# Kernel optimization log

Measured on AMD Instinct MI355X. Metric: run time of the kernel, lower is better.

## Reference

```python
import jax, jax.numpy as jnp
import numpy as np

N_HEAD = 16
ROPE_BASE = 10000.0


def _rope_tables(T, head_dim, dtype):
    inv_freq = 1.0 / (ROPE_BASE ** (jnp.arange(0, head_dim, 2, dtype=jnp.float32) / head_dim))
    t = jnp.arange(T, dtype=jnp.float32)
    freqs = t[:, None] * inv_freq[None, :]          # [T, hd/2]
    emb = jnp.concatenate([freqs, freqs], axis=-1)  # [T, hd]
    return jnp.cos(emb).astype(dtype), jnp.sin(emb).astype(dtype)


def _rotate_half(x):
    h = x.shape[-1] // 2
    return jnp.concatenate([-x[..., h:], x[..., :h]], axis=-1)


def setup_inputs() -> dict:
    key = jax.random.key(0)
    k1, k2, k3 = jax.random.split(key, 3)
    B, T, C = 2, 2048, 1024
    x = jax.random.normal(k1, (B, T, C), dtype=jnp.float32)
    w_attn = jax.random.normal(k2, (3 * C, C), dtype=jnp.float32) * (1.0 / np.sqrt(C))
    w_proj = jax.random.normal(k3, (C, C), dtype=jnp.float32) * (1.0 / np.sqrt(C))
    return {"x": x, "w_attn": w_attn, "w_proj": w_proj}


def reference(x, w_attn, w_proj):
    B, T, C = x.shape
    H = N_HEAD
    hd = C // H

    qkv = jnp.einsum('btc,fc->btf', x, w_attn)          # [B,T,3C]
    q, k, v = jnp.split(qkv, 3, axis=-1)
    # [B,H,T,hd]
    q = q.reshape(B, T, H, hd).transpose(0, 2, 1, 3)
    k = k.reshape(B, T, H, hd).transpose(0, 2, 1, 3)
    v = v.reshape(B, T, H, hd).transpose(0, 2, 1, 3)

    cos, sin = _rope_tables(T, hd, x.dtype)             # [T,hd]
    cos = cos[None, None]
    sin = sin[None, None]
    q = q * cos + _rotate_half(q) * sin
    k = k * cos + _rotate_half(k) * sin

    scale = 1.0 / np.sqrt(hd)
    scores = jnp.einsum('bhqd,bhkd->bhqk', q, k) * scale  # [B,H,T,T]
    causal = jnp.tril(jnp.ones((T, T), dtype=bool))
    scores = jnp.where(causal[None, None], scores, jnp.finfo(scores.dtype).min)
    attn = jax.nn.softmax(scores, axis=-1)
    out = jnp.einsum('bhqk,bhkd->bhqd', attn, v)          # [B,H,T,hd]
    out = out.transpose(0, 2, 1, 3).reshape(B, T, C)
    return jnp.einsum('btc,oc->bto', out, w_proj)
```

## Files before the change

kernel.cpp:

```cpp
#include <hip/hip_runtime.h>
#include <hip/hip_bf16.h>
#include <stdint.h>

typedef unsigned short u16;
typedef __bf16 bf16x8 __attribute__((ext_vector_type(8)));
typedef float f32x4 __attribute__((ext_vector_type(4)));

#define B_ 2
#define T_ 2048
#define C_ 1024
#define H_ 16
#define HD 64
#define M_ (B_ * T_)
#define N3 (3 * C_)

__device__ __forceinline__ float bf2f(u16 u) {
  return __uint_as_float(((unsigned int)u) << 16);
}
__device__ __forceinline__ u16 f2bf(float f) {
  unsigned int u = __float_as_uint(f);
  u += 0x7FFF + ((u >> 16) & 1);
  return (u16)(u >> 16);
}
__device__ __forceinline__ unsigned cvt_pk_bf16(float lo, float hi) {
  unsigned r;
  asm("v_cvt_pk_bf16_f32 %0, %1, %2" : "=v"(r) : "v"(lo), "v"(hi));
  return r;
}
__device__ __forceinline__ void async16(void* ldsp, const void* gp) {
  __builtin_amdgcn_global_load_lds(
      (const __attribute__((address_space(1))) unsigned int*)gp,
      (__attribute__((address_space(3))) unsigned int*)ldsp, 16, 0, 0);
}

union U16x8 { uint4 v; u16 u[8]; };

__device__ __forceinline__ bf16x8 ldsAfrag(const char* base, int row, int kbyte) {
  int off = (row * 128 + kbyte) ^ ((row & 7) << 4);
  uint4 t = *reinterpret_cast<const uint4*>(base + off);
  return __builtin_bit_cast(bf16x8, t);
}
__device__ __forceinline__ bf16x8 ldsAfrag256(const char* base, int row, int kbyte) {
  int off = (row * 256 + kbyte) ^ ((row & 7) << 4);
  uint4 t = *reinterpret_cast<const uint4*>(base + off);
  return __builtin_bit_cast(bf16x8, t);
}

__global__ void cvt_bf16(const float* __restrict__ src, u16* __restrict__ dst, int n4) {
  int i = blockIdx.x * blockDim.x + threadIdx.x;
  int stride = gridDim.x * blockDim.x;
  for (; i < n4; i += stride) {
    float4 v = reinterpret_cast<const float4*>(src)[i];
    uint2 o;
    o.x = (unsigned)f2bf(v.x) | ((unsigned)f2bf(v.y) << 16);
    o.y = (unsigned)f2bf(v.z) | ((unsigned)f2bf(v.w) << 16);
    reinterpret_cast<uint2*>(dst)[i] = o;
  }
}

__global__ void rope_tables_kernel(float* __restrict__ cosT, float* __restrict__ sinT) {
  int t = blockIdx.x;
  int i = threadIdx.x;
  float inv = powf(10000.0f, -(float)i * (1.0f / 32.0f));
  float f = (float)t * inv;
  cosT[t * 32 + i] = cosf(f);
  sinT[t * 32 + i] = sinf(f);
}

template <bool OUT_F32>
__global__ __launch_bounds__(256) void gemm_bt(const u16* __restrict__ A,
                                               const u16* __restrict__ Bw,
                                               void* __restrict__ Cout,
                                               int M, int N, int K) {
  __shared__ uint4 ldsbuf[2048];
  char* As = (char*)ldsbuf;
  char* Bs = (char*)ldsbuf + 16384;
  const int tid = threadIdx.x;
  const int lane = tid & 63;
  const int wv = tid >> 6;
  const int wr = wv >> 1, wc = wv & 1;
  const int lrow = lane & 15, lgrp = lane >> 4;
  const long m0 = (long)blockIdx.x * 128, n0 = (long)blockIdx.y * 128;
  const int srow = tid >> 3, sc = tid & 7;
  f32x4 acc[4][4] = {};
  for (int k0 = 0; k0 < K; k0 += 64) {
    __syncthreads();
#pragma unroll
    for (int p = 0; p < 4; ++p) {
      int row = srow + p * 32;
      uint4 va = *reinterpret_cast<const uint4*>(A + (m0 + row) * K + k0 + sc * 8);
      *reinterpret_cast<uint4*>(As + ((row * 128 + sc * 16) ^ ((row & 7) << 4))) = va;
      uint4 vb = *reinterpret_cast<const uint4*>(Bw + (n0 + row) * K + k0 + sc * 8);
      *reinterpret_cast<uint4*>(Bs + ((row * 128 + sc * 16) ^ ((row & 7) << 4))) = vb;
    }
    __syncthreads();
#pragma unroll
    for (int ks = 0; ks < 2; ++ks) {
      bf16x8 af[4], bfr[4];
#pragma unroll
      for (int i = 0; i < 4; ++i) {
        af[i]  = ldsAfrag(As, wr * 64 + i * 16 + lrow, ks * 64 + lgrp * 16);
        bfr[i] = ldsAfrag(Bs, wc * 64 + i * 16 + lrow, ks * 64 + lgrp * 16);
      }
#pragma unroll
      for (int i = 0; i < 4; ++i)
#pragma unroll
        for (int j = 0; j < 4; ++j)
          acc[i][j] = __builtin_amdgcn_mfma_f32_16x16x32_bf16(af[i], bfr[j], acc[i][j], 0, 0, 0);
    }
  }
#pragma unroll
  for (int i = 0; i < 4; ++i)
#pragma unroll
    for (int j = 0; j < 4; ++j) {
      long r0 = m0 + wr * 64 + i * 16 + lgrp * 4;
      long c  = n0 + wc * 64 + j * 16 + lrow;
#pragma unroll
      for (int r = 0; r < 4; ++r) {
        float v = acc[i][j][r];
        if (OUT_F32)
          ((float*)Cout)[(r0 + r) * N + c] = v;
        else
          ((u16*)Cout)[(r0 + r) * N + c] = f2bf(v);
      }
    }
}

__global__ __launch_bounds__(256) void rope_reshape(const u16* __restrict__ qkv,
                                                    const float* __restrict__ cosT,
                                                    const float* __restrict__ sinT,
                                                    u16* __restrict__ Q,
                                                    u16* __restrict__ K,
                                                    u16* __restrict__ Vt) {
  __shared__ u16 Vs[64][80];
  const int tid = threadIdx.x;
  const int tblk = blockIdx.x, bh = blockIdx.y;
  const int b = bh >> 4, h = bh & 15;
  const int tl = tid >> 2, quar = tid & 3;
  const int t = tblk * 64 + tl;
  const u16* rowp = qkv + ((size_t)(b * T_ + t)) * N3 + h * HD;
  const int d0 = quar * 8;
  float cs[8], sn[8];
#pragma unroll
  for (int j = 0; j < 8; ++j) {
    cs[j] = cosT[t * 32 + d0 + j];
    sn[j] = sinT[t * 32 + d0 + j];
  }
#pragma unroll
  for (int part = 0; part < 2; ++part) {
    const u16* p = rowp + part * C_;
    U16x8 x1, x2, o1, o2;
    x1.v = *reinterpret_cast<const uint4*>(p + d0);
    x2.v = *reinterpret_cast<const uint4*>(p + d0 + 32);
#pragma unroll
    for (int j = 0; j < 8; ++j) {
      float a = bf2f(x1.u[j]), c2 = bf2f(x2.u[j]);
      o1.u[j] = f2bf(a * cs[j] - c2 * sn[j]);
      o2.u[j] = f2bf(c2 * cs[j] + a * sn[j]);
    }
    u16* dst = (part ? K : Q) + ((size_t)bh * T_ + t) * HD;
    *reinterpret_cast<uint4*>(dst + d0) = o1.v;
    *reinterpret_cast<uint4*>(dst + d0 + 32) = o2.v;
  }
  const u16* pv = rowp + 2 * C_;
#pragma unroll
  for (int c = 0; c < 2; ++c) {
    int d = quar * 16 + c * 8;
    *reinterpret_cast<uint4*>(&Vs[tl][d]) = *reinterpret_cast<const uint4*>(pv + d);
  }
  __syncthreads();
  const int d = tid >> 2, tq = tid & 3;
  U16x8 a, bv;
#pragma unroll
  for (int j = 0; j < 8; ++j) a.u[j] = Vs[tq * 16 + j][d];
#pragma unroll
  for (int j = 0; j < 8; ++j) bv.u[j] = Vs[tq * 16 + 8 + j][d];
  u16* dstv = Vt + ((size_t)bh * HD + d) * T_ + tblk * 64 + tq * 16;
  *reinterpret_cast<uint4*>(dstv) = a.v;
  *reinterpret_cast<uint4*>(dstv + 8) = bv.v;
}

__global__ __launch_bounds__(256) void attn_fwd7(const u16* __restrict__ Q,
                                                 const u16* __restrict__ K,
                                                 const u16* __restrict__ Vt,
                                                 u16* __restrict__ O) {
  __shared__ uint4 lds4[5120];
  char* ldsb = (char*)lds4;
  const int tid = threadIdx.x;
  const int lane = tid & 63, wv = tid >> 6;
  const int lrow = lane & 15, lgrp = lane >> 4;
  char* Ps = ldsb + 65536 + wv * 4096;
  const int bh = blockIdx.y;
  const int b = bh >> 4, h = bh & 15;
  const u16* Qh = Q + (size_t)bh * T_ * HD;
  const u16* Kh = K + (size_t)bh * T_ * HD;
  const u16* Vh = Vt + (size_t)bh * HD * T_;

  const int kc_src = ((lane & 7) ^ (lane >> 3)) * 8;
  const int krow_l = lane >> 3;
  const int vrow_l = lane >> 4;

  auto stage = [&](int bufsel, int k0s) {
    char* Kd = ldsb + (bufsel << 15);
    char* Vd = Kd + 16384;
    const u16* Kg = Kh + (size_t)k0s * HD;
    const u16* Vg = Vh + k0s;
#pragma unroll
    for (int seg = 0; seg < 4; ++seg) {
      const u16* gk = Kg + (size_t)(wv * 32 + seg * 8 + krow_l) * HD + kc_src;
      async16(Kd + wv * 4096 + seg * 1024, gk);
      int d = wv * 16 + seg * 4 + vrow_l;
      const u16* gv = Vg + (size_t)d * T_ + ((lane & 15) ^ (d & 7)) * 8;
      async16(Vd + wv * 4096 + seg * 1024, gv);
    }
  };

  const float SCL = 0.125f * 1.44269504089f;
  const float CBIAS = 16.0f;
  uint4 ones4;
  ones4.x = ones4.y = ones4.z = ones4.w = 0x3F803F80u;
  const bf16x8 ones8 = __builtin_bit_cast(bf16x8, ones4);
  int cur = 0;

#pragma unroll
  for (int uu = 0; uu < 2; ++uu) {
    const int unit = uu ? (31 - (int)blockIdx.x) : (int)blockIdx.x;
    const int qs = unit * 64;
    const int q_glob = qs + wv * 16 + lrow;
    bf16x8 qf[2];
#pragma unroll
    for (int ks = 0; ks < 2; ++ks) {
      uint4 t4 = *reinterpret_cast<const uint4*>(
          Qh + (size_t)(qs + wv * 16 + lrow) * HD + ks * 32 + lgrp * 8);
      qf[ks] = __builtin_bit_cast(bf16x8, t4);
    }
    f32x4 o[4] = {};
    f32x4 lacc = {};
    const int niter = (unit >> 1) + 1;

    stage(cur, 0);
    __syncthreads();

    for (int kt = 0; kt < niter; ++kt) {
      const int k0 = kt * 128;
      if (kt + 1 < niter) stage(cur ^ 1, k0 + 128);
      char* Ksb = ldsb + (cur << 15);
      char* Vsb = Ksb + 16384;

      f32x4 s[8] = {};
      __builtin_amdgcn_s_setprio(1);
#pragma unroll
      for (int ks = 0; ks < 2; ++ks)
#pragma unroll
        for (int n = 0; n < 8; ++n) {
          bf16x8 bk = ldsAfrag(Ksb, n * 16 + lrow, ks * 64 + lgrp * 16);
          s[n] = __builtin_amdgcn_mfma_f32_16x16x32_bf16(bk, qf[ks], s[n], 0, 0, 0);
        }
      __builtin_amdgcn_s_setprio(0);

      const bool diag = (kt == niter - 1);
#pragma unroll
      for (int n = 0; n < 8; ++n)
#pragma unroll
        for (int r = 0; r < 4; ++r) {
          float v = __builtin_fmaf(s[n][r], SCL, -CBIAS);
          if (diag) {
            int kg = k0 + n * 16 + lgrp * 4 + r;
            v = (kg <= q_glob) ? v : -__builtin_inff();
          }
          s[n][r] = exp2f(v);
        }

#pragma unroll
      for (int n = 0; n < 8; ++n) {
        uint2 w;
        w.x = cvt_pk_bf16(s[n][0], s[n][1]);
        w.y = cvt_pk_bf16(s[n][2], s[n][3]);
        int off = (lrow * 256 + n * 32 + lgrp * 8) ^ ((lrow & 7) << 4);
        *reinterpret_cast<uint2*>(Ps + off) = w;
      }

      __builtin_amdgcn_s_setprio(1);
#pragma unroll
      for (int ks = 0; ks < 4; ++ks) {
        bf16x8 pa = ldsAfrag256(Ps, lrow, ks * 64 + lgrp * 16);
        lacc = __builtin_amdgcn_mfma_f32_16x16x32_bf16(pa, ones8, lacc, 0, 0, 0);
#pragma unroll
        for (int dn = 0; dn < 4; ++dn) {
          bf16x8 bv = ldsAfrag256(Vsb, dn * 16 + lrow, ks * 64 + lgrp * 16);
          o[dn] = __builtin_amdgcn_mfma_f32_16x16x32_bf16(pa, bv, o[dn], 0, 0, 0);
        }
      }
      __builtin_amdgcn_s_setprio(0);
      __syncthreads();
      cur ^= 1;
    }

#pragma unroll
    for (int r = 0; r < 4; ++r) {
      float inv = 1.0f / lacc[r];
      int t = qs + wv * 16 + lgrp * 4 + r;
#pragma unroll
      for (int dn = 0; dn < 4; ++dn) {
        int c = h * HD + dn * 16 + lrow;
        O[((size_t)(b * T_ + t)) * C_ + c] = f2bf(o[dn][r] * inv);
      }
    }
  }
}

extern "C" void kernel_launch(void* const* d_in, const int* in_sizes, int n_in,
                              void* d_out, int out_size, void* d_ws, size_t ws_size,
                              hipStream_t stream) {
  const float* x  = (const float*)d_in[0];
  const float* wa = (const float*)d_in[1];
  const float* wp = (const float*)d_in[2];
  float* out = (float*)d_out;
  char* ws = (char*)d_ws;
  size_t off = 0;
  auto alloc = [&](size_t bytes) {
    char* p = ws + off;
    off += (bytes + 255) & ~(size_t)255;
    return p;
  };
  u16* xb   = (u16*)alloc((size_t)M_ * C_ * 2);
  u16* wab  = (u16*)alloc((size_t)N3 * C_ * 2);
  u16* wpb  = (u16*)alloc((size_t)C_ * C_ * 2);
  u16* qkvb = (u16*)alloc((size_t)M_ * N3 * 2);
  u16* Qb   = (u16*)alloc((size_t)B_ * H_ * T_ * HD * 2);
  u16* Kb   = (u16*)alloc((size_t)B_ * H_ * T_ * HD * 2);
  u16* Vtb  = (u16*)alloc((size_t)B_ * H_ * T_ * HD * 2);
  u16* Ob   = (u16*)alloc((size_t)M_ * C_ * 2);
  float* cosT = (float*)alloc((size_t)T_ * 32 * 4);
  float* sinT = (float*)alloc((size_t)T_ * 32 * 4);
  (void)in_sizes; (void)n_in; (void)out_size; (void)ws_size;

  cvt_bf16<<<1024, 256, 0, stream>>>(x, xb, M_ * C_ / 4);
  cvt_bf16<<<1024, 256, 0, stream>>>(wa, wab, N3 * C_ / 4);
  cvt_bf16<<<512, 256, 0, stream>>>(wp, wpb, C_ * C_ / 4);
  rope_tables_kernel<<<T_, 32, 0, stream>>>(cosT, sinT);
  gemm_bt<false><<<dim3(M_ / 128, N3 / 128), 256, 0, stream>>>(xb, wab, qkvb, M_, N3, C_);
  rope_reshape<<<dim3(T_ / 64, B_ * H_), 256, 0, stream>>>(qkvb, cosT, sinT, Qb, Kb, Vtb);
  attn_fwd7<<<dim3(16, B_ * H_), 256, 0, stream>>>(Qb, Kb, Vtb, Ob);
  gemm_bt<true><<<dim3(M_ / 128, C_ / 128), 256, 0, stream>>>(Ob, wpb, out, M_, C_, C_);
}
```

Baseline: 131.5 us.

## Use async LDS loads in GEMM, fold softmax scale into Q, precompute attention LDS addresses

After: 128.0 us. 1.03x faster.

```diff
diff --git a/kernel.cpp b/kernel.cpp
--- a/kernel.cpp
+++ b/kernel.cpp
@@ -40,9 +40,8 @@
   uint4 t = *reinterpret_cast<const uint4*>(base + off);
   return __builtin_bit_cast(bf16x8, t);
 }
-__device__ __forceinline__ bf16x8 ldsAfrag256(const char* base, int row, int kbyte) {
-  int off = (row * 256 + kbyte) ^ ((row & 7) << 4);
-  uint4 t = *reinterpret_cast<const uint4*>(base + off);
+__device__ __forceinline__ bf16x8 ldsRead(const char* p) {
+  uint4 t = *reinterpret_cast<const uint4*>(p);
   return __builtin_bit_cast(bf16x8, t);
 }
 
@@ -81,17 +80,17 @@
   const int wr = wv >> 1, wc = wv & 1;
   const int lrow = lane & 15, lgrp = lane >> 4;
   const long m0 = (long)blockIdx.x * 128, n0 = (long)blockIdx.y * 128;
-  const int srow = tid >> 3, sc = tid & 7;
+  const int srow_l = lane >> 3;
+  const int csrc = ((lane & 7) ^ (lane >> 3)) * 8;
   f32x4 acc[4][4] = {};
   for (int k0 = 0; k0 < K; k0 += 64) {
     __syncthreads();
 #pragma unroll
     for (int p = 0; p < 4; ++p) {
-      int row = srow + p * 32;
-      uint4 va = *reinterpret_cast<const uint4*>(A + (m0 + row) * K + k0 + sc * 8);
-      *reinterpret_cast<uint4*>(As + ((row * 128 + sc * 16) ^ ((row & 7) << 4))) = va;
-      uint4 vb = *reinterpret_cast<const uint4*>(Bw + (n0 + row) * K + k0 + sc * 8);
-      *reinterpret_cast<uint4*>(Bs + ((row * 128 + sc * 16) ^ ((row & 7) << 4))) = vb;
+      int seg = wv * 4 + p;
+      int row = seg * 8 + srow_l;
+      async16(As + seg * 1024, A + (size_t)(m0 + row) * K + k0 + csrc);
+      async16(Bs + seg * 1024, Bw + (size_t)(n0 + row) * K + k0 + csrc);
     }
     __syncthreads();
 #pragma unroll
@@ -133,6 +132,7 @@
                                                     u16* __restrict__ K,
                                                     u16* __restrict__ Vt) {
   __shared__ u16 Vs[64][80];
+  const float SCLQ = 0.125f * 1.4426950408889634f;
   const int tid = threadIdx.x;
   const int tblk = blockIdx.x, bh = blockIdx.y;
   const int b = bh >> 4, h = bh & 15;
@@ -155,8 +155,11 @@
 #pragma unroll
     for (int j = 0; j < 8; ++j) {
       float a = bf2f(x1.u[j]), c2 = bf2f(x2.u[j]);
-      o1.u[j] = f2bf(a * cs[j] - c2 * sn[j]);
-      o2.u[j] = f2bf(c2 * cs[j] + a * sn[j]);
+      float f1 = a * cs[j] - c2 * sn[j];
+      float f2 = c2 * cs[j] + a * sn[j];
+      if (part == 0) { f1 *= SCLQ; f2 *= SCLQ; }
+      o1.u[j] = f2bf(f1);
+      o2.u[j] = f2bf(f2);
     }
     u16* dst = (part ? K : Q) + ((size_t)bh * T_ + t) * HD;
     *reinterpret_cast<uint4*>(dst + d0) = o1.v;
@@ -180,7 +183,7 @@
   *reinterpret_cast<uint4*>(dstv + 8) = bv.v;
 }
 
-__global__ __launch_bounds__(256) void attn_fwd7(const u16* __restrict__ Q,
+__global__ __launch_bounds__(256) void attn_fwd8(const u16* __restrict__ Q,
                                                  const u16* __restrict__ K,
                                                  const u16* __restrict__ Vt,
                                                  u16* __restrict__ O) {
@@ -215,8 +218,18 @@
     }
   };
 
-  const float SCL = 0.125f * 1.44269504089f;
-  const float CBIAS = 16.0f;
+  const int swz = (lrow & 7) << 4;
+  const int kread_a = lrow * 128 + ((lgrp * 16) ^ swz);
+  const int kread_b = lrow * 128 + ((64 + lgrp * 16) ^ swz);
+  const int vread_a = 16384 + lrow * 256 + ((lgrp * 16) ^ swz);
+  const int vread_b = 16384 + lrow * 256 + ((64 + lgrp * 16) ^ swz);
+  const char* pa_a = Ps + lrow * 256 + ((lgrp * 16) ^ swz);
+  const char* pa_b = Ps + lrow * 256 + ((64 + lgrp * 16) ^ swz);
+  char* pw0 = Ps + lrow * 256 + (((0 * 32 + lgrp * 8)) ^ swz);
+  char* pw1 = Ps + lrow * 256 + (((1 * 32 + lgrp * 8)) ^ swz);
+  char* pw2 = Ps + lrow * 256 + (((2 * 32 + lgrp * 8)) ^ swz);
+  char* pw3 = Ps + lrow * 256 + (((3 * 32 + lgrp * 8)) ^ swz);
+
   uint4 ones4;
   ones4.x = ones4.y = ones4.z = ones4.w = 0x3F803F80u;
   const bf16x8 ones8 = __builtin_bit_cast(bf16x8, ones4);
@@ -244,50 +257,58 @@
     for (int kt = 0; kt < niter; ++kt) {
       const int k0 = kt * 128;
       if (kt + 1 < niter) stage(cur ^ 1, k0 + 128);
-      char* Ksb = ldsb + (cur << 15);
-      char* Vsb = Ksb + 16384;
+      const char* Kb = ldsb + (cur << 15);
+      const char* KbA = Kb + kread_a;
+      const char* KbB = Kb + kread_b;
+      const char* VbA = Kb + vread_a;
+      const char* VbB = Kb + vread_b;
 
       f32x4 s[8] = {};
       __builtin_amdgcn_s_setprio(1);
 #pragma unroll
-      for (int ks = 0; ks < 2; ++ks)
-#pragma unroll
-        for (int n = 0; n < 8; ++n) {
-          bf16x8 bk = ldsAfrag(Ksb, n * 16 + lrow, ks * 64 + lgrp * 16);
-          s[n] = __builtin_amdgcn_mfma_f32_16x16x32_bf16(bk, qf[ks], s[n], 0, 0, 0);
-        }
+      for (int n = 0; n < 8; ++n)
+        s[n] = __builtin_amdgcn_mfma_f32_16x16x32_bf16(ldsRead(KbA + n * 2048), qf[0], s[n], 0, 0, 0);
+#pragma unroll
+      for (int n = 0; n < 8; ++n)
+        s[n] = __builtin_amdgcn_mfma_f32_16x16x32_bf16(ldsRead(KbB + n * 2048), qf[1], s[n], 0, 0, 0);
       __builtin_amdgcn_s_setprio(0);
 
       const bool diag = (kt == niter - 1);
-#pragma unroll
-      for (int n = 0; n < 8; ++n)
-#pragma unroll
-        for (int r = 0; r < 4; ++r) {
-          float v = __builtin_fmaf(s[n][r], SCL, -CBIAS);
-          if (diag) {
+      if (diag) {
+#pragma unroll
+        for (int n = 0; n < 8; ++n)
+#pragma unroll
+          for (int r = 0; r < 4; ++r) {
             int kg = k0 + n * 16 + lgrp * 4 + r;
-            v = (kg <= q_glob) ? v : -__builtin_inff();
+            float v = (kg <= q_glob) ? s[n][r] : -__builtin_inff();
+            s[n][r] = exp2f(v);
           }
-          s[n][r] = exp2f(v);
-        }
+      } else {
+#pragma unroll
+        for (int n = 0; n < 8; ++n)
+#pragma unroll
+          for (int r = 0; r < 4; ++r) s[n][r] = exp2f(s[n][r]);
+      }
 
 #pragma unroll
       for (int n = 0; n < 8; ++n) {
         uint2 w;
         w.x = cvt_pk_bf16(s[n][0], s[n][1]);
         w.y = cvt_pk_bf16(s[n][2], s[n][3]);
-        int off = (lrow * 256 + n * 32 + lgrp * 8) ^ ((lrow & 7) << 4);
-        *reinterpret_cast<uint2*>(Ps + off) = w;
+        char* pwb = (n & 3) == 0 ? pw0 : (n & 3) == 1 ? pw1 : (n & 3) == 2 ? pw2 : pw3;
+        *reinterpret_cast<uint2*>(pwb + (n >> 2) * 128) = w;
       }
 
       __builtin_amdgcn_s_setprio(1);
 #pragma unroll
       for (int ks = 0; ks < 4; ++ks) {
-        bf16x8 pa = ldsAfrag256(Ps, lrow, ks * 64 + lgrp * 16);
+        const char* pab = (ks & 1) ? pa_b : pa_a;
+        const char* vbb = (ks & 1) ? VbB : VbA;
+        bf16x8 pa = ldsRead(pab + (ks >> 1) * 128);
         lacc = __builtin_amdgcn_mfma_f32_16x16x32_bf16(pa, ones8, lacc, 0, 0, 0);
 #pragma unroll
         for (int dn = 0; dn < 4; ++dn) {
-          bf16x8 bv = ldsAfrag256(Vsb, dn * 16 + lrow, ks * 64 + lgrp * 16);
+          bf16x8 bv = ldsRead(vbb + dn * 4096 + (ks >> 1) * 128);
           o[dn] = __builtin_amdgcn_mfma_f32_16x16x32_bf16(pa, bv, o[dn], 0, 0, 0);
         }
       }
@@ -341,6 +362,6 @@
   rope_tables_kernel<<<T_, 32, 0, stream>>>(cosT, sinT);
   gemm_bt<false><<<dim3(M_ / 128, N3 / 128), 256, 0, stream>>>(xb, wab, qkvb, M_, N3, C_);
   rope_reshape<<<dim3(T_ / 64, B_ * H_), 256, 0, stream>>>(qkvb, cosT, sinT, Qb, Kb, Vtb);
-  attn_fwd7<<<dim3(16, B_ * H_), 256, 0, stream>>>(Qb, Kb, Vtb, Ob);
+  attn_fwd8<<<dim3(16, B_ * H_), 256, 0, stream>>>(Qb, Kb, Vtb, Ob);
   gemm_bt<true><<<dim3(M_ / 128, C_ / 128), 256, 0, stream>>>(Ob, wpb, out, M_, C_, C_);
 }
```
